# Performance work log

Measured on AMD Instinct MI355X. Metric: run time of the kernel, lower is better.

Reference implementation:

```python
import jax, jax.numpy as jnp
import numpy as np

N_NODES = 50000


def _sage_conv(x, src, dst, w_l, b_l, w_r):
    """PyG SAGEConv with mean aggregation: lin_l(mean_j x_j) + lin_r(x_i)."""
    msg = x[src]  # [E, d] gather from source nodes
    agg = jax.ops.segment_sum(msg, dst, num_segments=N_NODES)  # [N, d]
    deg = jax.ops.segment_sum(jnp.ones(dst.shape, dtype=x.dtype), dst, num_segments=N_NODES)
    agg = agg / jnp.maximum(deg, 1.0)[:, None]  # mean, zero-degree safe
    return agg @ w_l + b_l + x @ w_r


def setup_inputs() -> dict:
    key = jax.random.key(0)
    ks = jax.random.split(key, 6)
    in_dim, hid, out = 128, 512, 40
    x = jax.random.normal(ks[0], (N_NODES, in_dim), dtype=jnp.float32)
    edge_index = jax.random.randint(ks[1], (2, 800000), 0, N_NODES, dtype=jnp.int64)
    s1 = 1.0 / np.sqrt(in_dim)
    s2 = 1.0 / np.sqrt(hid)
    return {
        "x": x,
        "edge_index": edge_index,
        "w1_l": jax.random.normal(ks[2], (in_dim, hid), dtype=jnp.float32) * s1,
        "b1": jnp.zeros((hid,), dtype=jnp.float32),
        "w1_r": jax.random.normal(ks[3], (in_dim, hid), dtype=jnp.float32) * s1,
        "w2_l": jax.random.normal(ks[4], (hid, out), dtype=jnp.float32) * s2,
        "b2": jnp.zeros((out,), dtype=jnp.float32),
        "w2_r": jax.random.normal(ks[5], (hid, out), dtype=jnp.float32) * s2,
    }


def reference(x, edge_index, w1_l, b1, w1_r, w2_l, b2, w2_r):
    src, dst = edge_index[0], edge_index[1]
    h = _sage_conv(x, src, dst, w1_l, b1, w1_r)
    h = jax.nn.relu(h)  # dropout is identity at inference
    h = _sage_conv(h, src, dst, w2_l, b2, w2_r)
    return jax.nn.log_softmax(h, axis=1)
```

## Files before the change

kernel.cpp:

```cpp
#include <hip/hip_runtime.h>
#include <math.h>

#define N_NODES 50000
#define N_EDGES 800000
#define IN_DIM 128
#define HID 512
#define OUT_DIM 40
#define NRANGE 8
#define RANGE_SZ ((N_NODES + NRANGE - 1) / NRANGE)
#define NCHUNK 250
#define PER_CHUNK 3200
#define CAP 64

typedef __attribute__((ext_vector_type(8))) short bf16x8;
typedef __attribute__((ext_vector_type(4))) float f32x4;
typedef __attribute__((ext_vector_type(4))) int i32x4;

__device__ __forceinline__ ushort f2bf(float f) {
    unsigned u = __float_as_uint(f);
    u += 0x7fff + ((u >> 16) & 1);
    return (ushort)(u >> 16);
}

__device__ __forceinline__ float bf2f(ushort u) {
    return __uint_as_float(((unsigned)u) << 16);
}

__device__ __forceinline__ void gload_lds16(const ushort* g, ushort* l) {
    __builtin_amdgcn_global_load_lds(
        (__attribute__((address_space(1))) void*)g,
        (__attribute__((address_space(3))) void*)l, 16, 0, 0);
}

__global__ void zero_ints(int* __restrict__ a, int n) {
    int i = blockIdx.x * blockDim.x + threadIdx.x;
    if (i < n) a[i] = 0;
}

__global__ void fill_csr_part(const int* __restrict__ src, const int* __restrict__ dst,
                              int* __restrict__ cursor, int* __restrict__ csr_src) {
    int range = blockIdx.x & (NRANGE - 1);
    int chunk = blockIdx.x >> 3;
    int lo = range * RANGE_SZ;
    int hi = lo + RANGE_SZ; if (hi > N_NODES) hi = N_NODES;
    int beg = chunk * PER_CHUNK;
    for (int e = beg + threadIdx.x * 4; e < beg + PER_CHUNK; e += 1024) {
        i32x4 d4 = __builtin_nontemporal_load((const i32x4*)(dst + e));
        i32x4 s4 = __builtin_nontemporal_load((const i32x4*)(src + e));
        if (d4.x >= lo && d4.x < hi) {
            int pos = atomicAdd(&cursor[d4.x], 1);
            if (pos < CAP) csr_src[d4.x * CAP + pos] = s4.x;
        }
        if (d4.y >= lo && d4.y < hi) {
            int pos = atomicAdd(&cursor[d4.y], 1);
            if (pos < CAP) csr_src[d4.y * CAP + pos] = s4.y;
        }
        if (d4.z >= lo && d4.z < hi) {
            int pos = atomicAdd(&cursor[d4.z], 1);
            if (pos < CAP) csr_src[d4.z * CAP + pos] = s4.z;
        }
        if (d4.w >= lo && d4.w < hi) {
            int pos = atomicAdd(&cursor[d4.w], 1);
            if (pos < CAP) csr_src[d4.w * CAP + pos] = s4.w;
        }
    }
}

__global__ void cvt_x(const float* __restrict__ x, ushort* __restrict__ abuf) {
    int i = blockIdx.x * blockDim.x + threadIdx.x;
    if (i >= N_NODES * 32) return;
    int n = i >> 5, q = i & 31;
    float4 v = *(const float4*)(x + (size_t)n * 128 + q * 4);
    ushort4 o;
    o.x = f2bf(v.x); o.y = f2bf(v.y); o.z = f2bf(v.z); o.w = f2bf(v.w);
    *(ushort4*)(abuf + (size_t)n * 256 + 128 + q * 4) = o;
}

__global__ void agg_x(const int* __restrict__ cursor,
                      const int* __restrict__ csr_src, ushort* __restrict__ abuf) {
    int wid = threadIdx.x >> 6;
    int lane = threadIdx.x & 63;
    int n = blockIdx.x * 4 + wid;
    if (n >= N_NODES) return;
    int d = cursor[n]; if (d > CAP) d = CAP;
    int beg = n * CAP, end = beg + d;
    int half = lane >> 5, l32 = lane & 31;
    const ushort* xb = abuf + 128;
    float a0 = 0, a1 = 0, a2 = 0, a3 = 0;
    float b0 = 0, b1 = 0, b2_ = 0, b3 = 0;
    int e = beg + half;
    for (; e + 2 < end; e += 4) {
        int s0 = csr_src[e], s1 = csr_src[e + 2];
        ushort4 v0 = *(const ushort4*)(xb + (size_t)s0 * 256 + l32 * 4);
        ushort4 v1 = *(const ushort4*)(xb + (size_t)s1 * 256 + l32 * 4);
        a0 += bf2f(v0.x); a1 += bf2f(v0.y); a2 += bf2f(v0.z); a3 += bf2f(v0.w);
        b0 += bf2f(v1.x); b1 += bf2f(v1.y); b2_ += bf2f(v1.z); b3 += bf2f(v1.w);
    }
    if (e < end) {
        int s = csr_src[e];
        ushort4 v = *(const ushort4*)(xb + (size_t)s * 256 + l32 * 4);
        a0 += bf2f(v.x); a1 += bf2f(v.y); a2 += bf2f(v.z); a3 += bf2f(v.w);
    }
    a0 += b0; a1 += b1; a2 += b2_; a3 += b3;
    a0 += __shfl_xor(a0, 32);
    a1 += __shfl_xor(a1, 32);
    a2 += __shfl_xor(a2, 32);
    a3 += __shfl_xor(a3, 32);
    if (d < 1) d = 1;
    float inv = 1.0f / (float)d;
    if (half == 0) {
        ushort4 o;
        o.x = f2bf(a0 * inv); o.y = f2bf(a1 * inv);
        o.z = f2bf(a2 * inv); o.w = f2bf(a3 * inv);
        *(ushort4*)(abuf + (size_t)n * 256 + l32 * 4) = o;
    }
}

__global__ void cvt_weights(const float* __restrict__ w1l, const float* __restrict__ w1r,
                            const float* __restrict__ w2l, const float* __restrict__ w2r,
                            ushort* __restrict__ wt, ushort* __restrict__ wt2) {
    int i = blockIdx.x * blockDim.x + threadIdx.x;
    if (i < 512 * 256) {
        int k = i >> 9, c = i & 511;
        float v = (k < 128) ? w1l[(size_t)k * 512 + c] : w1r[(size_t)(k - 128) * 512 + c];
        wt[(size_t)c * 256 + k] = f2bf(v);
    } else if (i < 512 * 256 + 80 * 512) {
        int j = i - 512 * 256;
        int c = j >> 9, k = j & 511;
        float v = (c < 40) ? w2l[(size_t)k * 40 + c] : w2r[(size_t)k * 40 + (c - 40)];
        wt2[(size_t)c * 512 + k] = f2bf(v);
    }
}

#define EPI_LD 136
__global__ __launch_bounds__(256) void gemm1_mfma(
    const ushort* __restrict__ A, const ushort* __restrict__ BT,
    const float* __restrict__ bias, ushort* __restrict__ h) {
    __shared__ ushort pool[128 * EPI_LD];
    ushort* As = pool;
    ushort* Bs = pool + 8192;
    int tid = threadIdx.x;
    int wave = tid >> 6, lane = tid & 63;
    int wm = wave >> 1, wn = wave & 1;
    int nwg = gridDim.x;
    int q = nwg >> 3, r = nwg & 7;
    int xcd = blockIdx.x & 7, pos = blockIdx.x >> 3;
    int base = (xcd < r) ? xcd * (q + 1) : r * (q + 1) + (xcd - r) * q;
    int id = base + pos;
    int row0 = (id >> 2) * 128;
    int col0 = (id & 3) * 128;

    f32x4 acc[4][4] = {};
    for (int kk = 0; kk < 256; kk += 64) {
        #pragma unroll
        for (int c = 0; c < 4; ++c) {
            int ch = wave + c * 4;
            int o = ch * 1024 + lane * 16;
            int row = o >> 7;
            int s = (o >> 4) & 7;
            int ssrc = s ^ (row & 7);
            int gr = row0 + row; if (gr > N_NODES - 1) gr = N_NODES - 1;
            gload_lds16(A + (size_t)gr * 256 + kk + (ssrc << 3), As + ch * 512);
            int gc = col0 + row;
            gload_lds16(BT + (size_t)gc * 256 + kk + (ssrc << 3), Bs + ch * 512);
        }
        __syncthreads();
        #pragma unroll
        for (int kc = 0; kc < 2; ++kc) {
            int sbase = kc * 4 + (lane >> 4);
            bf16x8 af[4], bfr[4];
            #pragma unroll
            for (int m = 0; m < 4; ++m) {
                int row = wm * 64 + m * 16 + (lane & 15);
                af[m] = *(const bf16x8*)(As + row * 64 + ((sbase ^ (row & 7)) << 3));
            }
            #pragma unroll
            for (int n = 0; n < 4; ++n) {
                int row = wn * 64 + n * 16 + (lane & 15);
                bfr[n] = *(const bf16x8*)(Bs + row * 64 + ((sbase ^ (row & 7)) << 3));
            }
            #pragma unroll
            for (int m = 0; m < 4; ++m)
                #pragma unroll
                for (int n = 0; n < 4; ++n)
                    acc[m][n] = __builtin_amdgcn_mfma_f32_16x16x32_bf16(af[m], bfr[n], acc[m][n], 0, 0, 0);
        }
        __syncthreads();
    }

    #pragma unroll
    for (int n = 0; n < 4; ++n) {
        int col_l = wn * 64 + n * 16 + (lane & 15);
        float b = bias[col0 + col_l];
        #pragma unroll
        for (int m = 0; m < 4; ++m) {
            #pragma unroll
            for (int j = 0; j < 4; ++j) {
                int row_l = wm * 64 + m * 16 + (lane >> 4) * 4 + j;
                pool[row_l * EPI_LD + col_l] = f2bf(fmaxf(acc[m][n][j] + b, 0.f));
            }
        }
    }
    __syncthreads();
    #pragma unroll
    for (int it = 0; it < 8; ++it) {
        int idx = tid + it * 256;
        int row = idx >> 4, ch = idx & 15;
        int grow = row0 + row;
        if (grow < N_NODES) {
            int4 v = *(const int4*)(pool + row * EPI_LD + ch * 8);
            *(int4*)(h + (size_t)grow * 512 + col0 + ch * 8) = v;
        }
    }
}

__global__ __launch_bounds__(256) void gemm2_mfma(
    const ushort* __restrict__ hbf, const ushort* __restrict__ wt2,
    ushort* __restrict__ p, float* __restrict__ r) {
    __shared__ ushort As[2][128 * 64];
    __shared__ ushort Bs[2][80 * 64];
    int tid = threadIdx.x;
    int wave = tid >> 6, lane = tid & 63;
    int row0 = blockIdx.x * 128;
    f32x4 acc[2][5] = {};

    auto stage = [&](int buf, int kk) {
        #pragma unroll
        for (int c = 0; c < 4; ++c) {
            int ch = wave + c * 4;
            int o = ch * 1024 + lane * 16;
            int row = o >> 7;
            int s = (o >> 4) & 7;
            int ssrc = s ^ (row & 7);
            int gr = row0 + row; if (gr > N_NODES - 1) gr = N_NODES - 1;
            gload_lds16(hbf + (size_t)gr * 512 + kk + (ssrc << 3), As[buf] + ch * 512);
        }
        for (int ch = wave; ch < 10; ch += 4) {
            int o = ch * 1024 + lane * 16;
            int row = o >> 7;
            int s = (o >> 4) & 7;
            int ssrc = s ^ (row & 7);
            gload_lds16(wt2 + (size_t)row * 512 + kk + (ssrc << 3), Bs[buf] + ch * 512);
        }
    };

    stage(0, 0);
    __syncthreads();
    #pragma unroll
    for (int t = 0; t < 8; ++t) {
        int cur = t & 1;
        if (t < 7) stage(cur ^ 1, (t + 1) * 64);
        #pragma unroll
        for (int kc = 0; kc < 2; ++kc) {
            int sbase = kc * 4 + (lane >> 4);
            bf16x8 af[2], bfr[5];
            #pragma unroll
            for (int m = 0; m < 2; ++m) {
                int row = wave * 32 + m * 16 + (lane & 15);
                af[m] = *(const bf16x8*)(As[cur] + row * 64 + ((sbase ^ (row & 7)) << 3));
            }
            #pragma unroll
            for (int n = 0; n < 5; ++n) {
                int row = n * 16 + (lane & 15);
                bfr[n] = *(const bf16x8*)(Bs[cur] + row * 64 + ((sbase ^ (row & 7)) << 3));
            }
            #pragma unroll
            for (int m = 0; m < 2; ++m)
                #pragma unroll
                for (int n = 0; n < 5; ++n)
                    acc[m][n] = __builtin_amdgcn_mfma_f32_16x16x32_bf16(af[m], bfr[n], acc[m][n], 0, 0, 0);
        }
        __syncthreads();
    }
    #pragma unroll
    for (int m = 0; m < 2; ++m) {
        #pragma unroll
        for (int j = 0; j < 4; ++j) {
            int grow = row0 + wave * 32 + m * 16 + (lane >> 4) * 4 + j;
            if (grow >= N_NODES) continue;
            #pragma unroll
            for (int n = 0; n < 5; ++n) {
                int col = n * 16 + (lane & 15);
                float v = acc[m][n][j];
                if (col < 40) p[(size_t)grow * 40 + col] = f2bf(v);
                else          r[(size_t)grow * 40 + (col - 40)] = v;
            }
        }
    }
}

__global__ void final_kernel(const ushort* __restrict__ p, const float* __restrict__ rr,
                             const float* __restrict__ b2,
                             const int* __restrict__ cursor, const int* __restrict__ csr_src,
                             float* __restrict__ out) {
    int wid = threadIdx.x >> 6;
    int lane = threadIdx.x & 63;
    int n = blockIdx.x * 4 + wid;
    if (n >= N_NODES) return;
    int d = cursor[n]; if (d > CAP) d = CAP;
    int beg = n * CAP, end = beg + d;
    float acc0 = 0.f, acc1 = 0.f, acc2 = 0.f, acc3 = 0.f;
    int e = beg;
    if (lane < OUT_DIM) {
        for (; e + 3 < end; e += 4) {
            int s0 = csr_src[e], s1 = csr_src[e + 1];
            int s2 = csr_src[e + 2], s3 = csr_src[e + 3];
            acc0 += bf2f(p[(size_t)s0 * OUT_DIM + lane]);
            acc1 += bf2f(p[(size_t)s1 * OUT_DIM + lane]);
            acc2 += bf2f(p[(size_t)s2 * OUT_DIM + lane]);
            acc3 += bf2f(p[(size_t)s3 * OUT_DIM + lane]);
        }
        for (; e < end; ++e)
            acc0 += bf2f(p[(size_t)csr_src[e] * OUT_DIM + lane]);
    }
    if (d < 1) d = 1;
    float inv = 1.0f / (float)d;
    float v = (lane < OUT_DIM)
                  ? ((acc0 + acc1 + acc2 + acc3) * inv + b2[lane] + rr[(size_t)n * OUT_DIM + lane])
                  : -INFINITY;
    float m = v;
    #pragma unroll
    for (int off = 32; off; off >>= 1) m = fmaxf(m, __shfl_xor(m, off));
    float ex = (lane < OUT_DIM) ? expf(v - m) : 0.f;
    float ssum = ex;
    #pragma unroll
    for (int off = 32; off; off >>= 1) ssum += __shfl_xor(ssum, off);
    if (lane < OUT_DIM) out[(size_t)n * OUT_DIM + lane] = (v - m) - logf(ssum);
}

extern "C" void kernel_launch(void* const* d_in, const int* in_sizes, int n_in,
                              void* d_out, int out_size, void* d_ws, size_t ws_size,
                              hipStream_t stream) {
    const float* x    = (const float*)d_in[0];
    const int*   edge = (const int*)d_in[1];
    const int*   srce = edge;
    const int*   dste = edge + N_EDGES;
    const float* w1l  = (const float*)d_in[2];
    const float* b1   = (const float*)d_in[3];
    const float* w1r  = (const float*)d_in[4];
    const float* w2l  = (const float*)d_in[5];
    const float* b2   = (const float*)d_in[6];
    const float* w2r  = (const float*)d_in[7];
    float* out = (float*)d_out;

    char* ws = (char*)d_ws;
    size_t off = 0;
    auto alloc = [&](size_t bytes) -> void* {
        void* ptr = ws + off;
        off = (off + bytes + 255) & ~(size_t)255;
        return ptr;
    };
    int* cursor  = (int*)alloc((size_t)N_NODES * 4);
    int* csr_src = (int*)alloc((size_t)N_NODES * CAP * 4);
    ushort* abuf = (ushort*)alloc((size_t)N_NODES * 256 * 2);
    ushort* wt   = (ushort*)alloc((size_t)512 * 256 * 2);
    ushort* wt2  = (ushort*)alloc((size_t)80 * 512 * 2);
    ushort* h    = (ushort*)alloc((size_t)N_NODES * HID * 2);
    ushort* p    = (ushort*)alloc((size_t)N_NODES * OUT_DIM * 2);
    float* rbuf  = (float*)alloc((size_t)N_NODES * OUT_DIM * 4);

    zero_ints<<<(N_NODES + 255) / 256, 256, 0, stream>>>(cursor, N_NODES);
    fill_csr_part<<<NRANGE * NCHUNK, 256, 0, stream>>>(srce, dste, cursor, csr_src);
    cvt_x<<<(N_NODES * 32 + 255) / 256, 256, 0, stream>>>(x, abuf);
    cvt_weights<<<(512 * 256 + 80 * 512 + 255) / 256, 256, 0, stream>>>(w1l, w1r, w2l, w2r, wt, wt2);
    agg_x<<<(N_NODES + 3) / 4, 256, 0, stream>>>(cursor, csr_src, abuf);
    gemm1_mfma<<<4 * ((N_NODES + 127) / 128), 256, 0, stream>>>(abuf, wt, b1, h);
    gemm2_mfma<<<(N_NODES + 127) / 128, 256, 0, stream>>>(h, wt2, p, rbuf);
    final_kernel<<<(N_NODES + 3) / 4, 256, 0, stream>>>(p, rbuf, b2, cursor, csr_src, out);
}
```

Measured before the change: 169.6 us.

## Fuse prep kernels into one launch and store CSR source indices as ushort

Merges the zeroing, x conversion and weight conversion kernels into a single prep launch that dispatches work by block-index range, removing two launches. The CSR neighbor list now stores source indices as 16-bit values, which halves the bytes written by fill_csr_part and read by the two aggregation kernels. Nontemporal loads of the edge arrays become plain loads. The ushort indices work only because N_NODES (50000) fits in 16 bits, so they would break for larger graphs.

```diff
diff --git a/kernel.cpp b/kernel.cpp
--- a/kernel.cpp
+++ b/kernel.cpp
@@ -12,6 +12,11 @@
 #define PER_CHUNK 3200
 #define CAP 64
 
+#define CVTX_BLKS 6250
+#define CVTW_BLKS 672
+#define ZERO_BLKS 196
+#define PREP_BLKS (CVTX_BLKS + CVTW_BLKS + ZERO_BLKS)
+
 typedef __attribute__((ext_vector_type(8))) short bf16x8;
 typedef __attribute__((ext_vector_type(4))) float f32x4;
 typedef __attribute__((ext_vector_type(4))) int i32x4;
@@ -32,52 +37,68 @@
         (__attribute__((address_space(3))) void*)l, 16, 0, 0);
 }
 
-__global__ void zero_ints(int* __restrict__ a, int n) {
-    int i = blockIdx.x * blockDim.x + threadIdx.x;
-    if (i < n) a[i] = 0;
+__global__ void prep(const float* __restrict__ x, ushort* __restrict__ abuf,
+                     const float* __restrict__ w1l, const float* __restrict__ w1r,
+                     const float* __restrict__ w2l, const float* __restrict__ w2r,
+                     ushort* __restrict__ wt, ushort* __restrict__ wt2,
+                     int* __restrict__ cursor) {
+    int b = blockIdx.x, t = threadIdx.x;
+    if (b < CVTX_BLKS) {
+        int i = b * 256 + t;
+        int n = i >> 5, q = i & 31;
+        float4 v = *(const float4*)(x + (size_t)n * 128 + q * 4);
+        ushort4 o;
+        o.x = f2bf(v.x); o.y = f2bf(v.y); o.z = f2bf(v.z); o.w = f2bf(v.w);
+        *(ushort4*)(abuf + (size_t)n * 256 + 128 + q * 4) = o;
+    } else if (b < CVTX_BLKS + CVTW_BLKS) {
+        int i = (b - CVTX_BLKS) * 256 + t;
+        if (i < 512 * 256) {
+            int k = i >> 9, c = i & 511;
+            float v = (k < 128) ? w1l[(size_t)k * 512 + c] : w1r[(size_t)(k - 128) * 512 + c];
+            wt[(size_t)c * 256 + k] = f2bf(v);
+        } else {
+            int j = i - 512 * 256;
+            int c = j >> 9, k = j & 511;
+            float v = (c < 40) ? w2l[(size_t)k * 40 + c] : w2r[(size_t)k * 40 + (c - 40)];
+            wt2[(size_t)c * 512 + k] = f2bf(v);
+        }
+    } else {
+        int i = (b - CVTX_BLKS - CVTW_BLKS) * 256 + t;
+        if (i < N_NODES) cursor[i] = 0;
+    }
 }
 
 __global__ void fill_csr_part(const int* __restrict__ src, const int* __restrict__ dst,
-                              int* __restrict__ cursor, int* __restrict__ csr_src) {
+                              int* __restrict__ cursor, ushort* __restrict__ csr) {
     int range = blockIdx.x & (NRANGE - 1);
     int chunk = blockIdx.x >> 3;
     int lo = range * RANGE_SZ;
     int hi = lo + RANGE_SZ; if (hi > N_NODES) hi = N_NODES;
     int beg = chunk * PER_CHUNK;
     for (int e = beg + threadIdx.x * 4; e < beg + PER_CHUNK; e += 1024) {
-        i32x4 d4 = __builtin_nontemporal_load((const i32x4*)(dst + e));
-        i32x4 s4 = __builtin_nontemporal_load((const i32x4*)(src + e));
+        i32x4 d4 = *(const i32x4*)(dst + e);
+        i32x4 s4 = *(const i32x4*)(src + e);
         if (d4.x >= lo && d4.x < hi) {
             int pos = atomicAdd(&cursor[d4.x], 1);
-            if (pos < CAP) csr_src[d4.x * CAP + pos] = s4.x;
+            if (pos < CAP) csr[d4.x * CAP + pos] = (ushort)s4.x;
         }
         if (d4.y >= lo && d4.y < hi) {
             int pos = atomicAdd(&cursor[d4.y], 1);
-            if (pos < CAP) csr_src[d4.y * CAP + pos] = s4.y;
+            if (pos < CAP) csr[d4.y * CAP + pos] = (ushort)s4.y;
         }
         if (d4.z >= lo && d4.z < hi) {
             int pos = atomicAdd(&cursor[d4.z], 1);
-            if (pos < CAP) csr_src[d4.z * CAP + pos] = s4.z;
+            if (pos < CAP) csr[d4.z * CAP + pos] = (ushort)s4.z;
         }
         if (d4.w >= lo && d4.w < hi) {
             int pos = atomicAdd(&cursor[d4.w], 1);
-            if (pos < CAP) csr_src[d4.w * CAP + pos] = s4.w;
-        }
-    }
-}
-
-__global__ void cvt_x(const float* __restrict__ x, ushort* __restrict__ abuf) {
-    int i = blockIdx.x * blockDim.x + threadIdx.x;
-    if (i >= N_NODES * 32) return;
-    int n = i >> 5, q = i & 31;
-    float4 v = *(const float4*)(x + (size_t)n * 128 + q * 4);
-    ushort4 o;
-    o.x = f2bf(v.x); o.y = f2bf(v.y); o.z = f2bf(v.z); o.w = f2bf(v.w);
-    *(ushort4*)(abuf + (size_t)n * 256 + 128 + q * 4) = o;
+            if (pos < CAP) csr[d4.w * CAP + pos] = (ushort)s4.w;
+        }
+    }
 }
 
 __global__ void agg_x(const int* __restrict__ cursor,
-                      const int* __restrict__ csr_src, ushort* __restrict__ abuf) {
+                      const ushort* __restrict__ csr, ushort* __restrict__ abuf) {
     int wid = threadIdx.x >> 6;
     int lane = threadIdx.x & 63;
     int n = blockIdx.x * 4 + wid;
@@ -90,14 +111,14 @@
     float b0 = 0, b1 = 0, b2_ = 0, b3 = 0;
     int e = beg + half;
     for (; e + 2 < end; e += 4) {
-        int s0 = csr_src[e], s1 = csr_src[e + 2];
+        int s0 = csr[e], s1 = csr[e + 2];
         ushort4 v0 = *(const ushort4*)(xb + (size_t)s0 * 256 + l32 * 4);
         ushort4 v1 = *(const ushort4*)(xb + (size_t)s1 * 256 + l32 * 4);
         a0 += bf2f(v0.x); a1 += bf2f(v0.y); a2 += bf2f(v0.z); a3 += bf2f(v0.w);
         b0 += bf2f(v1.x); b1 += bf2f(v1.y); b2_ += bf2f(v1.z); b3 += bf2f(v1.w);
     }
     if (e < end) {
-        int s = csr_src[e];
+        int s = csr[e];
         ushort4 v = *(const ushort4*)(xb + (size_t)s * 256 + l32 * 4);
         a0 += bf2f(v.x); a1 += bf2f(v.y); a2 += bf2f(v.z); a3 += bf2f(v.w);
     }
@@ -113,22 +134,6 @@
         o.x = f2bf(a0 * inv); o.y = f2bf(a1 * inv);
         o.z = f2bf(a2 * inv); o.w = f2bf(a3 * inv);
         *(ushort4*)(abuf + (size_t)n * 256 + l32 * 4) = o;
-    }
-}
-
-__global__ void cvt_weights(const float* __restrict__ w1l, const float* __restrict__ w1r,
-                            const float* __restrict__ w2l, const float* __restrict__ w2r,
-                            ushort* __restrict__ wt, ushort* __restrict__ wt2) {
-    int i = blockIdx.x * blockDim.x + threadIdx.x;
-    if (i < 512 * 256) {
-        int k = i >> 9, c = i & 511;
-        float v = (k < 128) ? w1l[(size_t)k * 512 + c] : w1r[(size_t)(k - 128) * 512 + c];
-        wt[(size_t)c * 256 + k] = f2bf(v);
-    } else if (i < 512 * 256 + 80 * 512) {
-        int j = i - 512 * 256;
-        int c = j >> 9, k = j & 511;
-        float v = (c < 40) ? w2l[(size_t)k * 40 + c] : w2r[(size_t)k * 40 + (c - 40)];
-        wt2[(size_t)c * 512 + k] = f2bf(v);
     }
 }
 
@@ -291,7 +296,7 @@
 
 __global__ void final_kernel(const ushort* __restrict__ p, const float* __restrict__ rr,
                              const float* __restrict__ b2,
-                             const int* __restrict__ cursor, const int* __restrict__ csr_src,
+                             const int* __restrict__ cursor, const ushort* __restrict__ csr,
                              float* __restrict__ out) {
     int wid = threadIdx.x >> 6;
     int lane = threadIdx.x & 63;
@@ -303,15 +308,15 @@
     int e = beg;
     if (lane < OUT_DIM) {
         for (; e + 3 < end; e += 4) {
-            int s0 = csr_src[e], s1 = csr_src[e + 1];
-            int s2 = csr_src[e + 2], s3 = csr_src[e + 3];
+            int s0 = csr[e], s1 = csr[e + 1];
+            int s2 = csr[e + 2], s3 = csr[e + 3];
             acc0 += bf2f(p[(size_t)s0 * OUT_DIM + lane]);
             acc1 += bf2f(p[(size_t)s1 * OUT_DIM + lane]);
             acc2 += bf2f(p[(size_t)s2 * OUT_DIM + lane]);
             acc3 += bf2f(p[(size_t)s3 * OUT_DIM + lane]);
         }
         for (; e < end; ++e)
-            acc0 += bf2f(p[(size_t)csr_src[e] * OUT_DIM + lane]);
+            acc0 += bf2f(p[(size_t)csr[e] * OUT_DIM + lane]);
     }
     if (d < 1) d = 1;
     float inv = 1.0f / (float)d;
@@ -351,7 +356,7 @@
         return ptr;
     };
     int* cursor  = (int*)alloc((size_t)N_NODES * 4);
-    int* csr_src = (int*)alloc((size_t)N_NODES * CAP * 4);
+    ushort* csr  = (ushort*)alloc((size_t)N_NODES * CAP * 2);
     ushort* abuf = (ushort*)alloc((size_t)N_NODES * 256 * 2);
     ushort* wt   = (ushort*)alloc((size_t)512 * 256 * 2);
     ushort* wt2  = (ushort*)alloc((size_t)80 * 512 * 2);
@@ -359,12 +364,10 @@
     ushort* p    = (ushort*)alloc((size_t)N_NODES * OUT_DIM * 2);
     float* rbuf  = (float*)alloc((size_t)N_NODES * OUT_DIM * 4);
 
-    zero_ints<<<(N_NODES + 255) / 256, 256, 0, stream>>>(cursor, N_NODES);
-    fill_csr_part<<<NRANGE * NCHUNK, 256, 0, stream>>>(srce, dste, cursor, csr_src);
-    cvt_x<<<(N_NODES * 32 + 255) / 256, 256, 0, stream>>>(x, abuf);
-    cvt_weights<<<(512 * 256 + 80 * 512 + 255) / 256, 256, 0, stream>>>(w1l, w1r, w2l, w2r, wt, wt2);
-    agg_x<<<(N_NODES + 3) / 4, 256, 0, stream>>>(cursor, csr_src, abuf);
+    prep<<<PREP_BLKS, 256, 0, stream>>>(x, abuf, w1l, w1r, w2l, w2r, wt, wt2, cursor);
+    fill_csr_part<<<NRANGE * NCHUNK, 256, 0, stream>>>(srce, dste, cursor, csr);
+    agg_x<<<(N_NODES + 3) / 4, 256, 0, stream>>>(cursor, csr, abuf);
     gemm1_mfma<<<4 * ((N_NODES + 127) / 128), 256, 0, stream>>>(abuf, wt, b1, h);
     gemm2_mfma<<<(N_NODES + 127) / 128, 256, 0, stream>>>(h, wt2, p, rbuf);
-    final_kernel<<<(N_NODES + 3) / 4, 256, 0, stream>>>(p, rbuf, b2, cursor, csr_src, out);
-}
+    final_kernel<<<(N_NODES + 3) / 4, 256, 0, stream>>>(p, rbuf, b2, cursor, csr, out);
+}
```

Measured after the change: 161.9 us. -4.5%, faster.
